# Kernel tuning notes

Hardware: AMD Instinct MI355X
Metric: run time of the kernel (lower is better)

The kernel has to match this reference:

```python
import jax, jax.numpy as jnp
import numpy as np

EPS = 1e-8

def real_sph_harm(u):
    # u: [..., 3] unit vectors; returns real spherical harmonics for degrees 0..3
    x, y, z = u[..., 0], u[..., 1], u[..., 2]
    x2, y2, z2 = x * x, y * y, z * z
    Y0 = 0.28209479 * jnp.ones_like(x)[..., None]                       # [..., 1]
    Y1 = 0.48860251 * jnp.stack([y, z, x], axis=-1)                     # [..., 3]
    Y2 = jnp.stack([
        1.09254843 * x * y,
        1.09254843 * y * z,
        0.31539157 * (3.0 * z2 - 1.0),
        1.09254843 * x * z,
        0.54627422 * (x2 - y2)], axis=-1)                               # [..., 5]
    Y3 = jnp.stack([
        0.59004359 * y * (3.0 * x2 - y2),
        2.89061144 * x * y * z,
        0.45704579 * y * (5.0 * z2 - 1.0),
        0.37317633 * z * (5.0 * z2 - 3.0),
        0.45704579 * x * (5.0 * z2 - 1.0),
        1.44530572 * z * (x2 - y2),
        0.59004359 * x * (x2 - 3.0 * y2)], axis=-1)                     # [..., 7]
    return [Y0, Y1, Y2, Y3]


def setup_inputs() -> dict:
    key = jax.random.key(0)
    ks = jax.random.split(key, 8)
    B, N, F_IN, C, L = 8, 256, 4, 32, 4
    F_OUT = L * C * 2  # 256
    D_OUT = 40
    H = 32  # radial MLP hidden
    s = 0.1
    return {
        "x": jax.random.normal(ks[0], (B, N, F_IN), jnp.float32),
        "Wq": jax.random.normal(ks[1], (F_IN, C), jnp.float32) * s,
        "Wk": jax.random.normal(ks[2], (F_IN, C), jnp.float32) * s,
        "Wv": jax.random.normal(ks[3], (L, F_IN, C), jnp.float32) * s,
        "Rw1": jax.random.normal(ks[4], (1, H), jnp.float32) * s,
        "Rb1": jnp.zeros((H,), jnp.float32),
        "Rw2": jax.random.normal(ks[5], (H, L * C), jnp.float32) * s,
        "Rb2": jnp.zeros((L * C,), jnp.float32),
        "fc1_w": jax.random.normal(ks[6], (F_OUT, F_OUT), jnp.float32) * s,
        "fc1_b": jnp.zeros((F_OUT,), jnp.float32),
        "ln_g": jnp.ones((F_OUT,), jnp.float32),
        "ln_b": jnp.zeros((F_OUT,), jnp.float32),
        "fc2_w": jax.random.normal(ks[7], (F_OUT, D_OUT), jnp.float32) * s,
        "fc2_b": jnp.zeros((D_OUT,), jnp.float32),
    }


def reference(x, Wq, Wk, Wv, Rw1, Rb1, Rw2, Rb2, fc1_w, fc1_b, ln_g, ln_b, fc2_w, fc2_b):
    B, N, _ = x.shape
    L, _, C = Wv.shape
    # --- basis and r (get_basis_and_r): all-pairs displacements from coords ---
    coords = x[..., :3]
    d = coords[:, None, :, :] - coords[:, :, None, :]          # [B, i, j, 3]
    r = jnp.sqrt(jnp.sum(d * d, axis=-1) + EPS)                # [B, i, j]
    u = d / r[..., None]
    Ys = real_sph_harm(u)                                      # list of [B,i,j,2l+1]
    # --- radial net: per-degree, per-channel radial weights ---
    h = jax.nn.relu(r[..., None] @ Rw1 + Rb1)                  # [B,i,j,H]
    R = (h @ Rw2 + Rb2).reshape(B, N, N, L, C)                 # [B,i,j,L,C]
    # --- SSO3Res: equivariant attention (degree-0 q/k, basis-weighted values) ---
    q = x @ Wq
    k = x @ Wk
    logits = jnp.einsum('bic,bjc->bij', q, k) / jnp.sqrt(jnp.asarray(C, x.dtype))
    alpha = jax.nn.softmax(logits, axis=-1)                    # [B,i,j]
    vals = jnp.einsum('bjf,lfc->lbjc', x, Wv)                  # [L,B,j,C]
    invs = []
    for l in range(L):
        # out_l[i,c,m] = sum_j alpha_ij * R_ij,c * Y_l,ij,m * v_j,c
        out_l = jnp.einsum('bij,bijc,bijm,bjc->bicm', alpha, R[..., l, :], Ys[l], vals[l])
        invs.append(jnp.sqrt(jnp.sum(out_l * out_l, axis=-1) + EPS))   # [B,i,C]
    inv = jnp.concatenate(invs, axis=-1)                       # [B, N, L*C]
    # --- invariant pooling: max + mean over points -> out fiber (L*C*2) ---
    pooled = jnp.concatenate([inv.max(axis=1), inv.mean(axis=1)], axis=-1)  # [B, 2*L*C]
    # --- FC head: Linear -> LayerNorm -> ReLU -> Linear ---
    h1 = pooled @ fc1_w + fc1_b
    mu = h1.mean(axis=-1, keepdims=True)
    var = h1.var(axis=-1, keepdims=True)
    h1 = (h1 - mu) / jnp.sqrt(var + 1e-5) * ln_g + ln_b
    h1 = jax.nn.relu(h1)
    return h1 @ fc2_w + fc2_b
```

## Files before the change

### kernel.cpp

```cpp
#include <hip/hip_runtime.h>
#include <hip/hip_bf16.h>

#define BB 8
#define NN 256
#define LC 128

typedef short short8 __attribute__((ext_vector_type(8)));
typedef float f32x4 __attribute__((ext_vector_type(4)));

union U8 { short8 s; unsigned u[4]; };

__device__ inline unsigned pkbf(float a, float b){
    __hip_bfloat162 h = __float22bfloat162_rn(make_float2(a, b));
    union { __hip_bfloat162 h2; unsigned u; } cv; cv.h2 = h; return cv.u;
}

__device__ inline void stage_aY(short* __restrict__ slab, int j, float a,
                                float dx, float dy, float dz, float r2)
{
    const float ir = rsqrtf(r2);
    const float ux = dx*ir, uy = dy*ir, uz = dz*ir;
    const float X2 = ux*ux, Y2 = uy*uy, Z2 = uz*uz;
    const float y0  = 0.28209479f;
    const float y1  = 0.48860251f*uy, y2 = 0.48860251f*uz, y3 = 0.48860251f*ux;
    const float y4  = 1.09254843f*ux*uy;
    const float y5  = 1.09254843f*uy*uz;
    const float y6  = 0.31539157f*(3.f*Z2 - 1.f);
    const float y7  = 1.09254843f*ux*uz;
    const float y8  = 0.54627422f*(X2 - Y2);
    const float y9  = 0.59004359f*uy*(3.f*X2 - Y2);
    const float y10 = 2.89061144f*ux*uy*uz;
    const float y11 = 0.45704579f*uy*(5.f*Z2 - 1.f);
    const float y12 = 0.37317633f*uz*(5.f*Z2 - 3.f);
    const float y13 = 0.45704579f*ux*(5.f*Z2 - 1.f);
    const float y14 = 1.44530572f*uz*(X2 - Y2);
    const float y15 = 0.59004359f*ux*(X2 - 3.f*Y2);
    #define ST2(mm, va, vb) { unsigned uu = pkbf((va)*a, (vb)*a); \
        slab[(mm)*264 + j] = (short)(uu & 0xffff); slab[(mm+1)*264 + j] = (short)(uu >> 16); }
    ST2(0,  y0,  y1)  ST2(2,  y2,  y3)
    ST2(4,  y4,  y5)  ST2(6,  y6,  y7)
    ST2(8,  y8,  y9)  ST2(10, y10, y11)
    ST2(12, y12, y13) ST2(14, y14, y15)
    #undef ST2
}

__global__ __launch_bounds__(256) void so3_main(
    const float* __restrict__ xg,
    const float* __restrict__ Wq,
    const float* __restrict__ Wk,
    const float* __restrict__ Wv,
    const float* __restrict__ Rw1,
    const float* __restrict__ Rb1,
    const float* __restrict__ Rw2,
    const float* __restrict__ Rb2,
    float* __restrict__ invg)
{
    const int tid = threadIdx.x;
    const int blk = blockIdx.x;
    const int b = blk >> 6;
    const int iq = blk & 63;
    const int rowbase = b * NN;
    const int lane = tid & 63;
    const int w = tid >> 6;
    const int n = lane & 15;
    const int g = lane >> 4;
    const int kbase = g * 8;
    const int i = iq*4 + w;

    __shared__ __align__(16) float xs[NN*4];
    __shared__ short xsbf[NN*4];
    __shared__ short aYs[4][16*264];
    __shared__ float asum[4][256];

    const float4 x4 = *(const float4*)&xg[(rowbase + tid)*4];
    *(float4*)&xs[tid*4] = x4;
    {
        uint2 xb;
        xb.x = pkbf(x4.x, x4.y);
        xb.y = pkbf(x4.z, x4.w);
        *(uint2*)&xsbf[tid*4] = xb;
    }
    const float4 xi = *(const float4*)&xg[(rowbase + i)*4];

    float md0, md1, md2, md3;
    {
        const int c = lane & 31;
        const float qc = xi.x*Wq[c] + xi.y*Wq[32+c] + xi.z*Wq[64+c] + xi.w*Wq[96+c];
        md0 = qc*Wk[c]; md1 = qc*Wk[32+c]; md2 = qc*Wk[64+c]; md3 = qc*Wk[96+c];
        #pragma unroll
        for (int off = 16; off >= 1; off >>= 1) {
            md0 += __shfl_xor(md0, off);
            md1 += __shfl_xor(md1, off);
            md2 += __shfl_xor(md2, off);
            md3 += __shfl_xor(md3, off);
        }
        const float lscale = 0.17677669529663687f;
        md0 *= lscale; md1 *= lscale; md2 *= lscale; md3 *= lscale;
    }

    __syncthreads();

    float r_reg[16], lgv[16];
    #pragma unroll
    for (int s = 0; s < 16; ++s) {
        const float4 xa = *(const float4*)&xs[(16*s + n)*4];
        const float ddx = xa.x - xi.x, ddy = xa.y - xi.y, ddz = xa.z - xi.z;
        const float r2 = ddx*ddx + ddy*ddy + ddz*ddz + 1e-8f;
        r_reg[s] = sqrtf(r2);
        lgv[s] = md0*xa.x + md1*xa.y + md2*xa.z + md3*xa.w;
    }

    float mx = lgv[0];
    #pragma unroll
    for (int s = 1; s < 16; ++s) mx = fmaxf(mx, lgv[s]);
    #pragma unroll
    for (int off = 1; off <= 8; off <<= 1) mx = fmaxf(mx, __shfl_xor(mx, off));
    float es = 0.f;
    float ev[16];
    #pragma unroll
    for (int s = 0; s < 16; ++s) { ev[s] = __expf(lgv[s] - mx); es += ev[s]; }
    #pragma unroll
    for (int off = 1; off <= 8; off <<= 1) es += __shfl_xor(es, off);
    const float invS = 1.0f / es;
    #pragma unroll
    for (int s = 0; s < 16; ++s) asum[w][16*s + n] = ev[s]*invS;

    asm volatile("s_waitcnt lgkmcnt(0)" ::: "memory");
    __builtin_amdgcn_sched_barrier(0);

    short* slab = &aYs[w][0];
    #pragma unroll
    for (int e = 0; e < 4; ++e) {
        const int j = 64*g + 16*e + n;
        const float a = asum[w][j];
        const float4 xa = *(const float4*)&xs[j*4];
        const float ddx = xa.x - xi.x, ddy = xa.y - xi.y, ddz = xa.z - xi.z;
        const float r2 = ddx*ddx + ddy*ddy + ddz*ddz + 1e-8f;
        stage_aY(slab, j, a, ddx, ddy, ddz, r2);
    }

    float rw1q[8], rb1q[8];
    #pragma unroll
    for (int q = 0; q < 8; ++q) { rw1q[q] = Rw1[kbase+q]; rb1q[q] = Rb1[kbase+q]; }

    asm volatile("s_waitcnt lgkmcnt(0)" ::: "memory");
    __builtin_amdgcn_sched_barrier(0);

    const int boff = n*264 + 4*g;
    const f32x4 vzero = {0.f, 0.f, 0.f, 0.f};

    #pragma unroll
    for (int h4 = 0; h4 < 2; ++h4) {
        short8 bfrag[4], bv[4];
        float rb2v[4];
        #pragma unroll
        for (int t4 = 0; t4 < 4; ++t4) {
            const int col = h4*64 + t4*16 + n;
            U8 bf;
            #pragma unroll
            for (int qq = 0; qq < 4; ++qq)
                bf.u[qq] = pkbf(Rw2[(kbase+2*qq)*LC + col], Rw2[(kbase+2*qq+1)*LC + col]);
            bfrag[t4] = bf.s;
            rb2v[t4] = Rb2[col];
            U8 z; z.u[0] = 0; z.u[1] = 0; z.u[2] = 0; z.u[3] = 0;
            if (g == 0) {
                const int l = (h4*64 + t4*16) >> 5;
                const int cc = (t4 & 1)*16 + n;
                z.u[0] = pkbf(Wv[l*128 + cc],      Wv[l*128 + 32 + cc]);
                z.u[1] = pkbf(Wv[l*128 + 64 + cc], Wv[l*128 + 96 + cc]);
            }
            bv[t4] = z.s;
        }

        f32x4 acc[4] = {};

        #pragma unroll
        for (int tt = 0; tt < 8; ++tt) {
            const int j0 = 32*tt;

            const uint2 blo = *(const uint2*)&slab[boff + j0];
            const uint2 bhi = *(const uint2*)&slab[boff + j0 + 16];
            U8 bf2;
            bf2.u[0] = blo.x; bf2.u[1] = blo.y; bf2.u[2] = bhi.x; bf2.u[3] = bhi.y;

            uint2 P[2][4];
            #pragma unroll
            for (int jh = 0; jh < 2; ++jh) {
                const float rj = r_reg[2*tt + jh];
                U8 af;
                #pragma unroll
                for (int qq = 0; qq < 4; ++qq) {
                    const float h0 = fmaxf(rj*rw1q[2*qq]   + rb1q[2*qq],   0.f);
                    const float h1 = fmaxf(rj*rw1q[2*qq+1] + rb1q[2*qq+1], 0.f);
                    af.u[qq] = pkbf(h0, h1);
                }
                U8 afV; afV.u[0] = 0; afV.u[1] = 0; afV.u[2] = 0; afV.u[3] = 0;
                if (g == 0) {
                    const uint2 xb = *(const uint2*)&xsbf[(j0 + 16*jh + n)*4];
                    afV.u[0] = xb.x; afV.u[1] = xb.y;
                }
                #pragma unroll
                for (int t4 = 0; t4 < 4; ++t4) {
                    f32x4 d  = __builtin_amdgcn_mfma_f32_16x16x32_bf16(af.s,  bfrag[t4], vzero, 0, 0, 0);
                    f32x4 vv = __builtin_amdgcn_mfma_f32_16x16x32_bf16(afV.s, bv[t4],    vzero, 0, 0, 0);
                    P[jh][t4].x = pkbf((d[0]+rb2v[t4])*vv[0], (d[1]+rb2v[t4])*vv[1]);
                    P[jh][t4].y = pkbf((d[2]+rb2v[t4])*vv[2], (d[3]+rb2v[t4])*vv[3]);
                }
            }

            #pragma unroll
            for (int t4 = 0; t4 < 4; ++t4) {
                U8 a2;
                a2.u[0] = P[0][t4].x; a2.u[1] = P[0][t4].y;
                a2.u[2] = P[1][t4].x; a2.u[3] = P[1][t4].y;
                acc[t4] = __builtin_amdgcn_mfma_f32_16x16x32_bf16(a2.s, bf2.s, acc[t4], 0, 0, 0);
            }
        }

        #pragma unroll
        for (int t4 = 0; t4 < 4; ++t4) {
            const int l = h4*2 + (t4 >> 1);
            const int lo = l*l, hi = l*l + 2*l;
            const bool valid = (n >= lo) && (n <= hi);
            f32x4 aq = acc[t4];
            float s0 = valid ? aq[0]*aq[0] : 0.f;
            float s1 = valid ? aq[1]*aq[1] : 0.f;
            float s2 = valid ? aq[2]*aq[2] : 0.f;
            float s3 = valid ? aq[3]*aq[3] : 0.f;
            #pragma unroll
            for (int off = 1; off <= 8; off <<= 1) {
                s0 += __shfl_xor(s0, off);
                s1 += __shfl_xor(s1, off);
                s2 += __shfl_xor(s2, off);
                s3 += __shfl_xor(s3, off);
            }
            const float sv = (n==0) ? s0 : ((n==1) ? s1 : ((n==2) ? s2 : s3));
            if (n < 4) asum[w][h4*64 + t4*16 + g*4 + n] = sv;
        }
    }

    asm volatile("s_waitcnt lgkmcnt(0)" ::: "memory");
    __builtin_amdgcn_sched_barrier(0);
    {
        const float v0 = asum[w][lane];
        const float v1 = asum[w][lane + 64];
        float* dst = &invg[(size_t)(rowbase + i)*LC];
        dst[lane]      = sqrtf(v0 + 1e-8f);
        dst[lane + 64] = sqrtf(v1 + 1e-8f);
    }
}

__global__ __launch_bounds__(128) void so3_pool(
    const float* __restrict__ invg,
    float* __restrict__ pmax_p,
    float* __restrict__ psum_p)
{
    const int blk = blockIdx.x;
    const int b = blk >> 3;
    const int chunk = blk & 7;
    const int t = threadIdx.x;
    const int ibase = b*NN + chunk*32;
    float mx = -1e30f, sm = 0.f;
    #pragma unroll 4
    for (int k = 0; k < 32; ++k) {
        const float v = invg[(size_t)(ibase + k)*LC + t];
        mx = fmaxf(mx, v);
        sm += v;
    }
    pmax_p[(size_t)blk*LC + t] = mx;
    psum_p[(size_t)blk*LC + t] = sm;
}

__global__ __launch_bounds__(512) void so3_post(
    const float* __restrict__ pmax_p,
    const float* __restrict__ psum_p,
    const float* __restrict__ fc1_w,
    const float* __restrict__ fc1_b,
    const float* __restrict__ ln_g,
    const float* __restrict__ ln_b,
    const float* __restrict__ fc2_w,
    const float* __restrict__ fc2_b,
    float* __restrict__ outg)
{
    const int b = blockIdx.x;
    const int t = threadIdx.x;
    __shared__ float pooled[256];
    __shared__ float pfc1[2][256];
    __shared__ float h1s[256];
    __shared__ float pf2[8][40];
    __shared__ float redA[8], redB[8];

    if (t < 128) {
        float m0 = pmax_p[(size_t)(b*8)*LC + t];
        #pragma unroll
        for (int k = 1; k < 8; ++k) m0 = fmaxf(m0, pmax_p[(size_t)(b*8 + k)*LC + t]);
        pooled[t] = m0;
    } else if (t < 256) {
        const int lc = t - 128;
        float s0 = psum_p[(size_t)(b*8)*LC + lc];
        #pragma unroll
        for (int k = 1; k < 8; ++k) s0 += psum_p[(size_t)(b*8 + k)*LC + lc];
        pooled[t] = s0 * (1.f/256.f);
    }
    __syncthreads();

    {
        const int o = t & 255, kh = t >> 8;
        float acc = 0.f;
        for (int k = kh*128; k < kh*128 + 128; ++k)
            acc += pooled[k] * fc1_w[k*256 + o];
        pfc1[kh][o] = acc;
    }
    __syncthreads();

    float hval = 0.f;
    if (t < 256) hval = pfc1[0][t] + pfc1[1][t] + fc1_b[t];

    const int lane = t & 63, wid = t >> 6;
    float s1 = (t < 256) ? hval : 0.f;
    float s2 = (t < 256) ? hval*hval : 0.f;
    #pragma unroll
    for (int off = 32; off >= 1; off >>= 1) {
        s1 += __shfl_xor(s1, off);
        s2 += __shfl_xor(s2, off);
    }
    if (lane == 0) { redA[wid] = s1; redB[wid] = s2; }
    __syncthreads();
    s1 = redA[0]+redA[1]+redA[2]+redA[3];
    s2 = redB[0]+redB[1]+redB[2]+redB[3];
    if (t < 256) {
        const float mu = s1 * (1.f/256.f);
        const float var = s2 * (1.f/256.f) - mu*mu;
        float v = (hval - mu) * rsqrtf(var + 1e-5f) * ln_g[t] + ln_b[t];
        h1s[t] = fmaxf(v, 0.f);
    }
    __syncthreads();

    if (t < 320) {
        const int o = t % 40, ks = t / 40;
        float acc = 0.f;
        for (int k = ks*32; k < ks*32 + 32; ++k)
            acc += h1s[k] * fc2_w[k*40 + o];
        pf2[ks][o] = acc;
    }
    __syncthreads();
    if (t < 40) {
        float o = fc2_b[t];
        #pragma unroll
        for (int ks = 0; ks < 8; ++ks) o += pf2[ks][t];
        outg[b*40 + t] = o;
    }
}

extern "C" void kernel_launch(void* const* d_in, const int* in_sizes, int n_in,
                              void* d_out, int out_size, void* d_ws, size_t ws_size,
                              hipStream_t stream) {
    const float* x     = (const float*)d_in[0];
    const float* Wq    = (const float*)d_in[1];
    const float* Wk    = (const float*)d_in[2];
    const float* Wv    = (const float*)d_in[3];
    const float* Rw1   = (const float*)d_in[4];
    const float* Rb1   = (const float*)d_in[5];
    const float* Rw2   = (const float*)d_in[6];
    const float* Rb2   = (const float*)d_in[7];
    const float* fc1_w = (const float*)d_in[8];
    const float* fc1_b = (const float*)d_in[9];
    const float* ln_g  = (const float*)d_in[10];
    const float* ln_b  = (const float*)d_in[11];
    const float* fc2_w = (const float*)d_in[12];
    const float* fc2_b = (const float*)d_in[13];
    float* out = (float*)d_out;

    float* ws = (float*)d_ws;
    float* invg   = ws;
    float* pmax_p = invg + BB*NN*LC;
    float* psum_p = pmax_p + BB*8*LC;

    so3_main<<<BB*64, 256, 0, stream>>>(x, Wq, Wk, Wv, Rw1, Rb1, Rw2, Rb2, invg);
    so3_pool<<<BB*8, 128, 0, stream>>>(invg, pmax_p, psum_p);
    so3_post<<<BB, 512, 0, stream>>>(pmax_p, psum_p, fc1_w, fc1_b, ln_g, ln_b, fc2_w, fc2_b, out);
}
```

Measured before the change: 37.42 us.

## Split each query row across two waves with shared softmax and staging

Each block now handles 2 query rows instead of 4, and each row is split across two waves. The two waves of a pair each compute half of the softmax and half of the aY staging, combine their max and sum through shared memory, and then each computes one half of the L*C output columns. The grid doubles to 1024 blocks, which gives more parallelism across CUs and halves the per-wave MFMA column work. In exchange it adds block-level syncs and duplicates the per-j radial MLP and value MFMAs across the wave pair.

```diff
diff --git a/kernel.cpp b/kernel.cpp
--- a/kernel.cpp
+++ b/kernel.cpp
@@ -57,20 +57,26 @@
 {
     const int tid = threadIdx.x;
     const int blk = blockIdx.x;
-    const int b = blk >> 6;
-    const int iq = blk & 63;
+    const int b = blk >> 7;
+    const int i0 = (blk & 127) << 1;
     const int rowbase = b * NN;
     const int lane = tid & 63;
     const int w = tid >> 6;
+    const int iw = w >> 1;
+    const int h = w & 1;
+    const int pw = w ^ 1;
     const int n = lane & 15;
     const int g = lane >> 4;
     const int kbase = g * 8;
-    const int i = iq*4 + w;
+    const int i = i0 + iw;
+    const int jb = h * 128;
 
     __shared__ __align__(16) float xs[NN*4];
     __shared__ short xsbf[NN*4];
-    __shared__ short aYs[4][16*264];
-    __shared__ float asum[4][256];
+    __shared__ short slab2[2][16*264];
+    __shared__ float r_sh[2][NN];
+    __shared__ float evs[2][NN];
+    __shared__ float pex[4][2];
 
     const float4 x4 = *(const float4*)&xg[(rowbase + tid)*4];
     *(float4*)&xs[tid*4] = x4;
@@ -100,153 +106,153 @@
 
     __syncthreads();
 
-    float r_reg[16], lgv[16];
-    #pragma unroll
-    for (int s = 0; s < 16; ++s) {
-        const float4 xa = *(const float4*)&xs[(16*s + n)*4];
-        const float ddx = xa.x - xi.x, ddy = xa.y - xi.y, ddz = xa.z - xi.z;
-        const float r2 = ddx*ddx + ddy*ddy + ddz*ddz + 1e-8f;
-        r_reg[s] = sqrtf(r2);
-        lgv[s] = md0*xa.x + md1*xa.y + md2*xa.z + md3*xa.w;
-    }
-
-    float mx = lgv[0];
-    #pragma unroll
-    for (int s = 1; s < 16; ++s) mx = fmaxf(mx, lgv[s]);
-    #pragma unroll
-    for (int off = 1; off <= 8; off <<= 1) mx = fmaxf(mx, __shfl_xor(mx, off));
-    float es = 0.f;
-    float ev[16];
-    #pragma unroll
-    for (int s = 0; s < 16; ++s) { ev[s] = __expf(lgv[s] - mx); es += ev[s]; }
-    #pragma unroll
-    for (int off = 1; off <= 8; off <<= 1) es += __shfl_xor(es, off);
-    const float invS = 1.0f / es;
-    #pragma unroll
-    for (int s = 0; s < 16; ++s) asum[w][16*s + n] = ev[s]*invS;
-
-    asm volatile("s_waitcnt lgkmcnt(0)" ::: "memory");
-    __builtin_amdgcn_sched_barrier(0);
-
-    short* slab = &aYs[w][0];
-    #pragma unroll
-    for (int e = 0; e < 4; ++e) {
-        const int j = 64*g + 16*e + n;
-        const float a = asum[w][j];
+    float mx, es;
+    {
+        float lgv[8];
+        #pragma unroll
+        for (int s = 0; s < 8; ++s) {
+            const int j = jb + 16*s + n;
+            const float4 xa = *(const float4*)&xs[j*4];
+            const float ddx = xa.x - xi.x, ddy = xa.y - xi.y, ddz = xa.z - xi.z;
+            const float r2 = ddx*ddx + ddy*ddy + ddz*ddz + 1e-8f;
+            r_sh[iw][j] = sqrtf(r2);
+            lgv[s] = md0*xa.x + md1*xa.y + md2*xa.z + md3*xa.w;
+        }
+        mx = lgv[0];
+        #pragma unroll
+        for (int s = 1; s < 8; ++s) mx = fmaxf(mx, lgv[s]);
+        #pragma unroll
+        for (int off = 1; off <= 8; off <<= 1) mx = fmaxf(mx, __shfl_xor(mx, off));
+        es = 0.f;
+        #pragma unroll
+        for (int s = 0; s < 8; ++s) {
+            const float e = __expf(lgv[s] - mx);
+            evs[iw][jb + 16*s + n] = e;
+            es += e;
+        }
+        #pragma unroll
+        for (int off = 1; off <= 8; off <<= 1) es += __shfl_xor(es, off);
+        if (lane == 0) { pex[w][0] = mx; pex[w][1] = es; }
+    }
+
+    __syncthreads();
+
+    const float mxp = pex[pw][0], esp = pex[pw][1];
+    const float M = fmaxf(mx, mxp);
+    const float S = es*__expf(mx - M) + esp*__expf(mxp - M);
+    const float scale = __expf(mx - M) / S;
+
+    short* slab = &slab2[iw][0];
+    #pragma unroll
+    for (int e = 0; e < 2; ++e) {
+        const int j = jb + 32*g + 16*e + n;
+        const float a = evs[iw][j] * scale;
         const float4 xa = *(const float4*)&xs[j*4];
         const float ddx = xa.x - xi.x, ddy = xa.y - xi.y, ddz = xa.z - xi.z;
         const float r2 = ddx*ddx + ddy*ddy + ddz*ddz + 1e-8f;
         stage_aY(slab, j, a, ddx, ddy, ddz, r2);
     }
 
+    float r_reg[16];
+    #pragma unroll
+    for (int s = 0; s < 16; ++s) r_reg[s] = r_sh[iw][16*s + n];
+
     float rw1q[8], rb1q[8];
     #pragma unroll
     for (int q = 0; q < 8; ++q) { rw1q[q] = Rw1[kbase+q]; rb1q[q] = Rb1[kbase+q]; }
 
-    asm volatile("s_waitcnt lgkmcnt(0)" ::: "memory");
-    __builtin_amdgcn_sched_barrier(0);
+    short8 bfrag[4], bv[4];
+    float rb2v[4];
+    #pragma unroll
+    for (int t4 = 0; t4 < 4; ++t4) {
+        const int col = h*64 + t4*16 + n;
+        U8 bf;
+        #pragma unroll
+        for (int qq = 0; qq < 4; ++qq)
+            bf.u[qq] = pkbf(Rw2[(kbase+2*qq)*LC + col], Rw2[(kbase+2*qq+1)*LC + col]);
+        bfrag[t4] = bf.s;
+        rb2v[t4] = Rb2[col];
+        U8 z; z.u[0] = 0; z.u[1] = 0; z.u[2] = 0; z.u[3] = 0;
+        if (g == 0) {
+            const int l = (h*64 + t4*16) >> 5;
+            const int cc = (t4 & 1)*16 + n;
+            z.u[0] = pkbf(Wv[l*128 + cc],      Wv[l*128 + 32 + cc]);
+            z.u[1] = pkbf(Wv[l*128 + 64 + cc], Wv[l*128 + 96 + cc]);
+        }
+        bv[t4] = z.s;
+    }
+
+    __syncthreads();
 
     const int boff = n*264 + 4*g;
     const f32x4 vzero = {0.f, 0.f, 0.f, 0.f};
-
-    #pragma unroll
-    for (int h4 = 0; h4 < 2; ++h4) {
-        short8 bfrag[4], bv[4];
-        float rb2v[4];
-        #pragma unroll
-        for (int t4 = 0; t4 < 4; ++t4) {
-            const int col = h4*64 + t4*16 + n;
-            U8 bf;
+    f32x4 acc[4] = {};
+
+    #pragma unroll
+    for (int tt = 0; tt < 8; ++tt) {
+        const int j0 = 32*tt;
+
+        const uint2 blo = *(const uint2*)&slab[boff + j0];
+        const uint2 bhi = *(const uint2*)&slab[boff + j0 + 16];
+        U8 bf2;
+        bf2.u[0] = blo.x; bf2.u[1] = blo.y; bf2.u[2] = bhi.x; bf2.u[3] = bhi.y;
+
+        uint2 P[2][4];
+        #pragma unroll
+        for (int jh = 0; jh < 2; ++jh) {
+            const float rj = r_reg[2*tt + jh];
+            U8 af;
             #pragma unroll
-            for (int qq = 0; qq < 4; ++qq)
-                bf.u[qq] = pkbf(Rw2[(kbase+2*qq)*LC + col], Rw2[(kbase+2*qq+1)*LC + col]);
-            bfrag[t4] = bf.s;
-            rb2v[t4] = Rb2[col];
-            U8 z; z.u[0] = 0; z.u[1] = 0; z.u[2] = 0; z.u[3] = 0;
+            for (int qq = 0; qq < 4; ++qq) {
+                const float h0 = fmaxf(rj*rw1q[2*qq]   + rb1q[2*qq],   0.f);
+                const float h1 = fmaxf(rj*rw1q[2*qq+1] + rb1q[2*qq+1], 0.f);
+                af.u[qq] = pkbf(h0, h1);
+            }
+            U8 afV; afV.u[0] = 0; afV.u[1] = 0; afV.u[2] = 0; afV.u[3] = 0;
             if (g == 0) {
-                const int l = (h4*64 + t4*16) >> 5;
-                const int cc = (t4 & 1)*16 + n;
-                z.u[0] = pkbf(Wv[l*128 + cc],      Wv[l*128 + 32 + cc]);
-                z.u[1] = pkbf(Wv[l*128 + 64 + cc], Wv[l*128 + 96 + cc]);
+                const uint2 xb = *(const uint2*)&xsbf[(j0 + 16*jh + n)*4];
+                afV.u[0] = xb.x; afV.u[1] = xb.y;
             }
-            bv[t4] = z.s;
-        }
-
-        f32x4 acc[4] = {};
-
-        #pragma unroll
-        for (int tt = 0; tt < 8; ++tt) {
-            const int j0 = 32*tt;
-
-            const uint2 blo = *(const uint2*)&slab[boff + j0];
-            const uint2 bhi = *(const uint2*)&slab[boff + j0 + 16];
-            U8 bf2;
-            bf2.u[0] = blo.x; bf2.u[1] = blo.y; bf2.u[2] = bhi.x; bf2.u[3] = bhi.y;
-
-            uint2 P[2][4];
-            #pragma unroll
-            for (int jh = 0; jh < 2; ++jh) {
-                const float rj = r_reg[2*tt + jh];
-                U8 af;
-                #pragma unroll
-                for (int qq = 0; qq < 4; ++qq) {
-                    const float h0 = fmaxf(rj*rw1q[2*qq]   + rb1q[2*qq],   0.f);
-                    const float h1 = fmaxf(rj*rw1q[2*qq+1] + rb1q[2*qq+1], 0.f);
-                    af.u[qq] = pkbf(h0, h1);
-                }
-                U8 afV; afV.u[0] = 0; afV.u[1] = 0; afV.u[2] = 0; afV.u[3] = 0;
-                if (g == 0) {
-                    const uint2 xb = *(const uint2*)&xsbf[(j0 + 16*jh + n)*4];
-                    afV.u[0] = xb.x; afV.u[1] = xb.y;
-                }
-                #pragma unroll
-                for (int t4 = 0; t4 < 4; ++t4) {
-                    f32x4 d  = __builtin_amdgcn_mfma_f32_16x16x32_bf16(af.s,  bfrag[t4], vzero, 0, 0, 0);
-                    f32x4 vv = __builtin_amdgcn_mfma_f32_16x16x32_bf16(afV.s, bv[t4],    vzero, 0, 0, 0);
-                    P[jh][t4].x = pkbf((d[0]+rb2v[t4])*vv[0], (d[1]+rb2v[t4])*vv[1]);
-                    P[jh][t4].y = pkbf((d[2]+rb2v[t4])*vv[2], (d[3]+rb2v[t4])*vv[3]);
-                }
-            }
-
             #pragma unroll
             for (int t4 = 0; t4 < 4; ++t4) {
-                U8 a2;
-                a2.u[0] = P[0][t4].x; a2.u[1] = P[0][t4].y;
-                a2.u[2] = P[1][t4].x; a2.u[3] = P[1][t4].y;
-                acc[t4] = __builtin_amdgcn_mfma_f32_16x16x32_bf16(a2.s, bf2.s, acc[t4], 0, 0, 0);
+                f32x4 d  = __builtin_amdgcn_mfma_f32_16x16x32_bf16(af.s,  bfrag[t4], vzero, 0, 0, 0);
+                f32x4 vv = __builtin_amdgcn_mfma_f32_16x16x32_bf16(afV.s, bv[t4],    vzero, 0, 0, 0);
+                P[jh][t4].x = pkbf((d[0]+rb2v[t4])*vv[0], (d[1]+rb2v[t4])*vv[1]);
+                P[jh][t4].y = pkbf((d[2]+rb2v[t4])*vv[2], (d[3]+rb2v[t4])*vv[3]);
             }
         }
 
         #pragma unroll
         for (int t4 = 0; t4 < 4; ++t4) {
-            const int l = h4*2 + (t4 >> 1);
-            const int lo = l*l, hi = l*l + 2*l;
-            const bool valid = (n >= lo) && (n <= hi);
-            f32x4 aq = acc[t4];
-            float s0 = valid ? aq[0]*aq[0] : 0.f;
-            float s1 = valid ? aq[1]*aq[1] : 0.f;
-            float s2 = valid ? aq[2]*aq[2] : 0.f;
-            float s3 = valid ? aq[3]*aq[3] : 0.f;
-            #pragma unroll
-            for (int off = 1; off <= 8; off <<= 1) {
-                s0 += __shfl_xor(s0, off);
-                s1 += __shfl_xor(s1, off);
-                s2 += __shfl_xor(s2, off);
-                s3 += __shfl_xor(s3, off);
-            }
-            const float sv = (n==0) ? s0 : ((n==1) ? s1 : ((n==2) ? s2 : s3));
-            if (n < 4) asum[w][h4*64 + t4*16 + g*4 + n] = sv;
-        }
-    }
-
-    asm volatile("s_waitcnt lgkmcnt(0)" ::: "memory");
-    __builtin_amdgcn_sched_barrier(0);
-    {
-        const float v0 = asum[w][lane];
-        const float v1 = asum[w][lane + 64];
-        float* dst = &invg[(size_t)(rowbase + i)*LC];
-        dst[lane]      = sqrtf(v0 + 1e-8f);
-        dst[lane + 64] = sqrtf(v1 + 1e-8f);
+            U8 a2;
+            a2.u[0] = P[0][t4].x; a2.u[1] = P[0][t4].y;
+            a2.u[2] = P[1][t4].x; a2.u[3] = P[1][t4].y;
+            acc[t4] = __builtin_amdgcn_mfma_f32_16x16x32_bf16(a2.s, bf2.s, acc[t4], 0, 0, 0);
+        }
+    }
+
+    #pragma unroll
+    for (int t4 = 0; t4 < 4; ++t4) {
+        const int l = h*2 + (t4 >> 1);
+        const int lo = l*l, hi = l*l + 2*l;
+        const bool valid = (n >= lo) && (n <= hi);
+        f32x4 aq = acc[t4];
+        float s0 = valid ? aq[0]*aq[0] : 0.f;
+        float s1 = valid ? aq[1]*aq[1] : 0.f;
+        float s2 = valid ? aq[2]*aq[2] : 0.f;
+        float s3 = valid ? aq[3]*aq[3] : 0.f;
+        #pragma unroll
+        for (int off = 1; off <= 8; off <<= 1) {
+            s0 += __shfl_xor(s0, off);
+            s1 += __shfl_xor(s1, off);
+            s2 += __shfl_xor(s2, off);
+            s3 += __shfl_xor(s3, off);
+        }
+        const float sv = (n==0) ? s0 : ((n==1) ? s1 : ((n==2) ? s2 : s3));
+        if (n < 4) {
+            const int col = h*64 + t4*16 + g*4 + n;
+            invg[(size_t)(rowbase + i)*LC + col] = sqrtf(sv + 1e-8f);
+        }
     }
 }
 
@@ -376,7 +382,7 @@
     float* pmax_p = invg + BB*NN*LC;
     float* psum_p = pmax_p + BB*8*LC;
 
-    so3_main<<<BB*64, 256, 0, stream>>>(x, Wq, Wk, Wv, Rw1, Rb1, Rw2, Rb2, invg);
+    so3_main<<<BB*128, 256, 0, stream>>>(x, Wq, Wk, Wv, Rw1, Rb1, Rw2, Rb2, invg);
     so3_pool<<<BB*8, 128, 0, stream>>>(invg, pmax_p, psum_p);
     so3_post<<<BB, 512, 0, stream>>>(pmax_p, psum_p, fc1_w, fc1_b, ln_g, ln_b, fc2_w, fc2_b, out);
 }
```

Result: slower. 39.62 us (+5.9%).
